# Kernel tuning notes

Hardware: AMD Instinct MI355X
Metric: run time of the kernel (lower is better)

The kernel has to match this reference:

```python
import jax, jax.numpy as jnp
import numpy as np


def setup_inputs() -> dict:
    key = jax.random.key(0)
    kq, kk, kv = jax.random.split(key, 3)
    B, H, L, D = 2, 16, 2048, 64
    Q = jax.random.normal(kq, (B, H, L, D), dtype=jnp.float32)
    K = jax.random.normal(kk, (B, H, L, D), dtype=jnp.float32)
    V = jax.random.normal(kv, (B, H, L, D), dtype=jnp.float32)
    return {"Q": Q, "K": K, "V": V, "topk": 64}


def reference(Q, K, V, topk):
    # dots = Q K^T : [B, H, Lq, Lk]
    dots = jnp.einsum("bhqd,bhkd->bhqk", Q, K)
    B, H, Lq, Lk = dots.shape
    # top-k sparsification along key axis, activation applied only to kept scores
    top_dots, top_inds = jax.lax.top_k(dots, topk)          # [B,H,Lq,topk]
    top_attn = jax.nn.softmax(top_dots, axis=-1)            # activation on top-k scores
    # scatter activated values back into a zero [B,H,Lq,Lk] matrix
    rows = jnp.arange(B * H * Lq)[:, None]
    attn = (
        jnp.zeros((B * H * Lq, Lk), dots.dtype)
        .at[rows, top_inds.reshape(-1, topk)]
        .set(top_attn.reshape(-1, topk))
        .reshape(B, H, Lq, Lk)
    )
    # out = attn V : [B, H, Lq, Dv]
    return jnp.einsum("bhqk,bhkv->bhqv", attn, V)
```

## Files before the change

kernel.cpp:

```cpp
#include <hip/hip_runtime.h>

typedef _Float16 half8_t __attribute__((ext_vector_type(8)));
typedef _Float16 half4_t __attribute__((ext_vector_type(4)));
typedef float    f32x4   __attribute__((ext_vector_type(4)));

#define LSEQ    2048
#define DIM     64
#define ROWS    16
#define TOPK    64
#define CAP     128
#define NROWTOT 65536

__global__ void cvt_f16_kernel(const float* __restrict__ Q, const float* __restrict__ K,
                               _Float16* __restrict__ Q16, _Float16* __restrict__ K16, int n4)
{
    int i = blockIdx.x * blockDim.x + threadIdx.x;
    if (i >= n4) return;
    float4 q = reinterpret_cast<const float4*>(Q)[i];
    float4 k = reinterpret_cast<const float4*>(K)[i];
    half4_t hq = { (_Float16)q.x, (_Float16)q.y, (_Float16)q.z, (_Float16)q.w };
    half4_t hk = { (_Float16)k.x, (_Float16)k.y, (_Float16)k.z, (_Float16)k.w };
    reinterpret_cast<half4_t*>(Q16)[i] = hq;
    reinterpret_cast<half4_t*>(K16)[i] = hk;
}

template <bool PRE>
__global__ __launch_bounds__(512, 4) void topk_attn_kernel(
    const float* __restrict__ Qf, const float* __restrict__ Kf, const float* __restrict__ Vf,
    const _Float16* __restrict__ Q16, const _Float16* __restrict__ K16,
    float* __restrict__ Out)
{
    __shared__ _Float16 sc[ROWS][LSEQ];
    __shared__ float    qlds[ROWS][DIM];
    __shared__ int      candIdx[8][CAP + 1];
    __shared__ int      pvK[8][TOPK];
    __shared__ float    pvW[8][TOPK];

    const int tid  = threadIdx.x;
    const int wave = tid >> 6;
    const int lane = tid & 63;

    const long rowbase  = (long)blockIdx.x * ROWS;
    const long headbase = (rowbase >> 11) << 11;

    for (int i = tid; i < ROWS * DIM; i += 512)
        qlds[i >> 6][i & 63] = Qf[rowbase * DIM + i];

    const int g = lane >> 4;
    const int r = lane & 15;

    half8_t a0, a1;
    if constexpr (PRE) {
        a0 = *reinterpret_cast<const half8_t*>(Q16 + (rowbase + r) * DIM + g * 8);
        a1 = *reinterpret_cast<const half8_t*>(Q16 + (rowbase + r) * DIM + 32 + g * 8);
    } else {
        const float* qp = Qf + (rowbase + r) * DIM + g * 8;
        #pragma unroll
        for (int j = 0; j < 8; ++j) { a0[j] = (_Float16)qp[j]; a1[j] = (_Float16)qp[32 + j]; }
    }

    #pragma unroll 4
    for (int t = 0; t < 16; ++t) {
        const int key = t * 128 + wave * 16 + r;
        half8_t b0, b1;
        if constexpr (PRE) {
            const _Float16* kp = K16 + (headbase + key) * DIM + g * 8;
            b0 = *reinterpret_cast<const half8_t*>(kp);
            b1 = *reinterpret_cast<const half8_t*>(kp + 32);
        } else {
            const float* kp = Kf + (headbase + key) * DIM + g * 8;
            #pragma unroll
            for (int j = 0; j < 8; ++j) { b0[j] = (_Float16)kp[j]; b1[j] = (_Float16)kp[32 + j]; }
        }
        f32x4 acc = {0.f, 0.f, 0.f, 0.f};
        acc = __builtin_amdgcn_mfma_f32_16x16x32_f16(a0, b0, acc, 0, 0, 0);
        acc = __builtin_amdgcn_mfma_f32_16x16x32_f16(a1, b1, acc, 0, 0, 0);
        #pragma unroll
        for (int j = 0; j < 4; ++j)
            sc[g * 4 + j][key] = (_Float16)acc[j];
    }
    __syncthreads();

    const unsigned long long mlt = (1ull << lane) - 1ull;

    for (int rr = 0; rr < 2; ++rr) {
        const int row = wave * 2 + rr;

        const half8_t* sp = reinterpret_cast<const half8_t*>(&sc[row][lane * 32]);
        half8_t h0 = sp[0], h1 = sp[1], h2 = sp[2], h3 = sp[3];
        float v[32];
        #pragma unroll
        for (int j = 0; j < 8; ++j) {
            v[j]      = (float)h0[j];
            v[8 + j]  = (float)h1[j];
            v[16 + j] = (float)h2[j];
            v[24 + j] = (float)h3[j];
        }

        float sm = 0.f, s2 = 0.f;
        #pragma unroll
        for (int j = 0; j < 32; ++j) {
            sm += v[j];
            s2 = fmaf(v[j], v[j], s2);
        }
        #pragma unroll
        for (int o = 32; o > 0; o >>= 1) {
            sm += __shfl_xor(sm, o);
            s2 += __shfl_xor(s2, o);
        }
        const float mu  = sm * (1.f / LSEQ);
        const float sig = sqrtf(fmaxf(s2 * (1.f / LSEQ) - mu * mu, 0.f));

        const float E2 = 0.30f;
        float T0  = mu + 1.60f * sig;
        float stp = 0.5f * sig + 0.05f;
        for (int it = 0; it < 16; ++it) {
            int ca = 0, ch = 0;
            #pragma unroll
            for (int j = 0; j < 32; ++j) {
                ca += (v[j] >= T0);
                ch += (v[j] > T0 + E2);
            }
            #pragma unroll
            for (int o = 32; o > 0; o >>= 1) {
                ca += __shfl_xor(ca, o);
                ch += __shfl_xor(ch, o);
            }
            if (ch >= TOPK && ca <= CAP) break;
            T0 += (ca > CAP) ? stp : -stp;
            stp *= 0.6f;
        }

        int myCnt = 0;
        #pragma unroll
        for (int j = 0; j < 32; ++j) myCnt += (v[j] >= T0);
        int pre = myCnt;
        #pragma unroll
        for (int o = 1; o < 64; o <<= 1) {
            int tu = __shfl_up(pre, o);
            if (lane >= o) pre += tu;
        }
        const int start = pre - myCnt;
        int nAll = __shfl(pre, 63);
        if (nAll > CAP) nAll = CAP;

        int cur = start;
        #pragma unroll
        for (int j = 0; j < 32; ++j) {
            const bool c = (v[j] >= T0);
            const int addr = (c && cur < CAP) ? cur : CAP;
            candIdx[wave][addr] = lane * 32 + j;
            cur += c;
        }
        asm volatile("s_waitcnt lgkmcnt(0)" ::: "memory");

        float ex[2]; unsigned us[2]; int ci[2];
        #pragma unroll
        for (int p = 0; p < 2; ++p) {
            const int c = lane + 64 * p;
            const bool valid = (c < nAll);
            const int key = valid ? candIdx[wave][c] : 0;
            ci[p] = key;
            float dot = 0.f;
            const float4* kp4 = reinterpret_cast<const float4*>(Kf + (headbase + key) * DIM);
            #pragma unroll
            for (int chk = 0; chk < 16; ++chk) {
                const float4 kk = kp4[chk];
                dot = fmaf(kk.x, qlds[row][chk * 4 + 0], dot);
                dot = fmaf(kk.y, qlds[row][chk * 4 + 1], dot);
                dot = fmaf(kk.z, qlds[row][chk * 4 + 2], dot);
                dot = fmaf(kk.w, qlds[row][chk * 4 + 3], dot);
            }
            ex[p] = dot;
            unsigned u = __float_as_uint(dot);
            u ^= (unsigned)((int)u >> 31) | 0x80000000u;
            us[p] = valid ? u : 0u;
        }

        unsigned cut = 0u;
        #pragma unroll
        for (int b = 31; b >= 0; --b) {
            const unsigned trial = cut | (1u << b);
            const int cnt = __popcll(__ballot(us[0] >= trial)) +
                            __popcll(__ballot(us[1] >= trial));
            if (cnt >= TOPK) cut = trial;
        }

        const unsigned long long beq0 = __ballot(us[0] == cut);
        const unsigned long long beq1 = __ballot(us[1] == cut);
        const int cntGt = __popcll(__ballot(us[0] > cut)) + __popcll(__ballot(us[1] > cut));
        const int need  = TOPK - cntGt;
        const int rank0 = __popcll(beq0 & mlt);
        const int rank1 = __popcll(beq0) + __popcll(beq1 & mlt);
        const bool sel0 = (us[0] > cut) || ((us[0] == cut) && (rank0 < need));
        const bool sel1 = (us[1] > cut) || ((us[1] == cut) && (rank1 < need));

        float mxe = fmaxf(sel0 ? ex[0] : -1e30f, sel1 ? ex[1] : -1e30f);
        #pragma unroll
        for (int o = 32; o > 0; o >>= 1) mxe = fmaxf(mxe, __shfl_xor(mxe, o));
        const float w0 = sel0 ? expf(ex[0] - mxe) : 0.f;
        const float w1 = sel1 ? expf(ex[1] - mxe) : 0.f;
        float zs = w0 + w1;
        #pragma unroll
        for (int o = 32; o > 0; o >>= 1) zs += __shfl_xor(zs, o);
        const float inv = 1.f / zs;

        pvK[wave][lane] = 0;
        pvW[wave][lane] = 0.f;
        const unsigned long long bs0 = __ballot(sel0);
        const unsigned long long bs1 = __ballot(sel1);
        const int pos0 = __popcll(bs0 & mlt);
        const int pos1 = __popcll(bs0) + __popcll(bs1 & mlt);
        if (sel0) { pvK[wave][pos0] = ci[0]; pvW[wave][pos0] = w0 * inv; }
        if (sel1) { pvK[wave][pos1] = ci[1]; pvW[wave][pos1] = w1 * inv; }
        asm volatile("s_waitcnt lgkmcnt(0)" ::: "memory");

        float acc = 0.f;
        #pragma unroll 16
        for (int i = 0; i < TOPK; ++i) {
            const int   ki = pvK[wave][i];
            const float wi = pvW[wave][i];
            acc = fmaf(wi, Vf[(headbase + ki) * DIM + lane], acc);
        }
        Out[(rowbase + row) * DIM + lane] = acc;
    }
}

extern "C" void kernel_launch(void* const* d_in, const int* in_sizes, int n_in,
                              void* d_out, int out_size, void* d_ws, size_t ws_size,
                              hipStream_t stream)
{
    const float* Q = (const float*)d_in[0];
    const float* K = (const float*)d_in[1];
    const float* V = (const float*)d_in[2];
    float* Out = (float*)d_out;

    const int nElem = 2 * 16 * 2048 * 64;
    const size_t needWs = (size_t)2 * (size_t)nElem * sizeof(_Float16);

    if (ws_size >= needWs) {
        _Float16* Q16 = (_Float16*)d_ws;
        _Float16* K16 = Q16 + nElem;
        cvt_f16_kernel<<<(nElem / 4) / 256, 256, 0, stream>>>(Q, K, Q16, K16, nElem / 4);
        topk_attn_kernel<true><<<NROWTOT / ROWS, 512, 0, stream>>>(Q, K, V, Q16, K16, Out);
    } else {
        topk_attn_kernel<false><<<NROWTOT / ROWS, 512, 0, stream>>>(Q, K, V, nullptr, nullptr, Out);
    }
}
```

Measured before the change: 684.2 us.

## Use wave ballots for threshold counting and candidate compaction in fp16

Keeps the per-lane scores packed as fp16 vectors instead of unpacking 32 floats, and compares them against an fp16-cast threshold. Counting and candidate compaction now use ballot and popcount instead of per-lane counts with shuffle reductions and a prefix scan. The LDS reads are XOR-permuted by lane to spread bank accesses, and the overflow slot in the candidate buffer is dropped. This cuts VGPR pressure and shuffle latency, but each bisection iteration now issues 64 ballots, and fp16 threshold rounding can change which candidates are kept near the boundary.

```diff
diff --git a/kernel.cpp b/kernel.cpp
--- a/kernel.cpp
+++ b/kernel.cpp
@@ -32,7 +32,7 @@
 {
     __shared__ _Float16 sc[ROWS][LSEQ];
     __shared__ float    qlds[ROWS][DIM];
-    __shared__ int      candIdx[8][CAP + 1];
+    __shared__ int      candIdx[8][CAP];
     __shared__ int      pvK[8][TOPK];
     __shared__ float    pvW[8][TOPK];
 
@@ -82,27 +82,27 @@
     __syncthreads();
 
     const unsigned long long mlt = (1ull << lane) - 1ull;
+    const int perm = lane & 3;
 
     for (int rr = 0; rr < 2; ++rr) {
         const int row = wave * 2 + rr;
 
         const half8_t* sp = reinterpret_cast<const half8_t*>(&sc[row][lane * 32]);
-        half8_t h0 = sp[0], h1 = sp[1], h2 = sp[2], h3 = sp[3];
-        float v[32];
-        #pragma unroll
-        for (int j = 0; j < 8; ++j) {
-            v[j]      = (float)h0[j];
-            v[8 + j]  = (float)h1[j];
-            v[16 + j] = (float)h2[j];
-            v[24 + j] = (float)h3[j];
-        }
+        half8_t h[4];
+        h[0] = sp[0 ^ perm];
+        h[1] = sp[1 ^ perm];
+        h[2] = sp[2 ^ perm];
+        h[3] = sp[3 ^ perm];
 
         float sm = 0.f, s2 = 0.f;
         #pragma unroll
-        for (int j = 0; j < 32; ++j) {
-            sm += v[j];
-            s2 = fmaf(v[j], v[j], s2);
-        }
+        for (int i = 0; i < 4; ++i)
+            #pragma unroll
+            for (int e = 0; e < 8; ++e) {
+                const float x = (float)h[i][e];
+                sm += x;
+                s2 = fmaf(x, x, s2);
+            }
         #pragma unroll
         for (int o = 32; o > 0; o >>= 1) {
             sm += __shfl_xor(sm, o);
@@ -115,43 +115,35 @@
         float T0  = mu + 1.60f * sig;
         float stp = 0.5f * sig + 0.05f;
         for (int it = 0; it < 16; ++it) {
+            const _Float16 hT  = (_Float16)T0;
+            const _Float16 hT2 = (_Float16)(T0 + E2);
             int ca = 0, ch = 0;
             #pragma unroll
-            for (int j = 0; j < 32; ++j) {
-                ca += (v[j] >= T0);
-                ch += (v[j] > T0 + E2);
-            }
-            #pragma unroll
-            for (int o = 32; o > 0; o >>= 1) {
-                ca += __shfl_xor(ca, o);
-                ch += __shfl_xor(ch, o);
-            }
+            for (int i = 0; i < 4; ++i)
+                #pragma unroll
+                for (int e = 0; e < 8; ++e) {
+                    ca += __popcll(__ballot(h[i][e] >= hT));
+                    ch += __popcll(__ballot(h[i][e] >  hT2));
+                }
             if (ch >= TOPK && ca <= CAP) break;
             T0 += (ca > CAP) ? stp : -stp;
             stp *= 0.6f;
         }
 
-        int myCnt = 0;
-        #pragma unroll
-        for (int j = 0; j < 32; ++j) myCnt += (v[j] >= T0);
-        int pre = myCnt;
-        #pragma unroll
-        for (int o = 1; o < 64; o <<= 1) {
-            int tu = __shfl_up(pre, o);
-            if (lane >= o) pre += tu;
-        }
-        const int start = pre - myCnt;
-        int nAll = __shfl(pre, 63);
-        if (nAll > CAP) nAll = CAP;
-
-        int cur = start;
-        #pragma unroll
-        for (int j = 0; j < 32; ++j) {
-            const bool c = (v[j] >= T0);
-            const int addr = (c && cur < CAP) ? cur : CAP;
-            candIdx[wave][addr] = lane * 32 + j;
-            cur += c;
-        }
+        const _Float16 hTf = (_Float16)T0;
+        int total = 0;
+        #pragma unroll
+        for (int i = 0; i < 4; ++i)
+            #pragma unroll
+            for (int e = 0; e < 8; ++e) {
+                const bool c = (h[i][e] >= hTf);
+                const unsigned long long b = __ballot(c);
+                const int pos = total + __popcll(b & mlt);
+                if (c && pos < CAP)
+                    candIdx[wave][pos] = lane * 32 + ((i ^ perm) << 3) + e;
+                total += __popcll(b);
+            }
+        int nAll = (total > CAP) ? CAP : total;
         asm volatile("s_waitcnt lgkmcnt(0)" ::: "memory");
 
         float ex[2]; unsigned us[2]; int ci[2];
```

New measurement: 1.049 ms. 1.53x slower.
